# Optimization experiments

Hardware: AMD Instinct MI355X
Metric: run time of the kernel (lower is better)

Reference implementation:

```python
import jax, jax.numpy as jnp
import numpy as np

DIM = 4096  # hadamard_dim, power of 2 -> K=1, pure FWHT with 1/sqrt(n) scaling


def fwht(x):
    """Fast Walsh-Hadamard transform along the last axis, normalized by 1/sqrt(n).

    Butterfly network: log2(n) stages of pairwise add/sub. Matches the math of
    multiplying by the normalized n x n Hadamard matrix (x @ H / sqrt(n)).
    """
    orig_shape = x.shape
    n = orig_shape[-1]
    x = x.reshape(-1, n)
    h = 1
    while h < n:  # static unrolled loop over log2(n) stages (n is static)
        # view as [rows, n/(2h), 2, h]; butterfly pairs are (s=0, s=1)
        xb = x.reshape(-1, n // (2 * h), 2, h)
        a = xb[:, :, 0, :]
        b = xb[:, :, 1, :]
        x = jnp.stack([a + b, a - b], axis=2).reshape(-1, n)
        h *= 2
    scale = jnp.asarray(1.0 / np.sqrt(n), dtype=x.dtype)
    return (x * scale).reshape(orig_shape)


def setup_inputs() -> dict:
    key = jax.random.key(0)
    x = jax.random.normal(key, (4, 2048, DIM), dtype=jnp.float32)
    return {"x": x}


def reference(x):
    # force_fp32=True path: compute in fp32 (x already fp32), cast back to input dtype
    x_dtype = x.dtype
    y = fwht(x.astype(jnp.float32))
    return y.astype(x_dtype)
```

## Files before the change

kernel.cpp:

```cpp
#include <hip/hip_runtime.h>


using v4 = __attribute__((ext_vector_type(4))) float;
using u2 = __attribute__((ext_vector_type(2))) unsigned;

__device__ __forceinline__ void bfly_perm32(float& x, float& y) {
    u2 r = __builtin_amdgcn_permlane32_swap(__float_as_uint(x), __float_as_uint(y),
                                            false, false);
    float u = __uint_as_float(r[0]), v = __uint_as_float(r[1]);
    float s = u + v, d = u - v;
    u2 r2 = __builtin_amdgcn_permlane32_swap(__float_as_uint(s), __float_as_uint(d),
                                             false, false);
    x = __uint_as_float(r2[0]); y = __uint_as_float(r2[1]);
}

__device__ __forceinline__ void bfly_perm16(float& x, float& y) {
    u2 r = __builtin_amdgcn_permlane16_swap(__float_as_uint(x), __float_as_uint(y),
                                            false, false);
    float u = __uint_as_float(r[0]), v = __uint_as_float(r[1]);
    float s = u + v, d = u - v;
    u2 r2 = __builtin_amdgcn_permlane16_swap(__float_as_uint(s), __float_as_uint(d),
                                             false, false);
    x = __uint_as_float(r2[0]); y = __uint_as_float(r2[1]);
}

__device__ __forceinline__ void had16(float x[16]) {
#pragma unroll
    for (int h = 1; h < 16; h <<= 1) {
#pragma unroll
        for (int i = 0; i < 16; ++i) {
            if (!(i & h)) {
                float a = x[i], b = x[i ^ h];
                x[i] = a + b; x[i ^ h] = a - b;
            }
        }
    }
}

__global__ void __launch_bounds__(256) fwht4096_kernel(const float* __restrict__ in,
                                                       float* __restrict__ out) {
    __shared__ float lds[4096];
    const int t = threadIdx.x;
    const size_t base = (size_t)blockIdx.x * 4096;
    const v4* in4 = reinterpret_cast<const v4*>(in + base);
    v4* out4 = reinterpret_cast<v4*>(out + base);

    v4 v[4];
#pragma unroll
    for (int j = 0; j < 4; ++j) v[j] = __builtin_nontemporal_load(&in4[t + 256 * j]);

#pragma unroll
    for (int j = 0; j < 4; ++j) {
        float a = v[j][0], b = v[j][1], c = v[j][2], d = v[j][3];
        float ab = a + b, amb = a - b, cd = c + d, cmd = c - d;
        v[j][0] = ab + cd; v[j][1] = amb + cmd; v[j][2] = ab - cd; v[j][3] = amb - cmd;
    }
    {
        v4 s0 = v[0] + v[1], d0 = v[0] - v[1];
        v4 s1 = v[2] + v[3], d1 = v[2] - v[3];
        v[0] = s0 + s1; v[2] = s0 - s1;
        v[1] = d0 + d1; v[3] = d0 - d1;
    }
    {
#pragma unroll
        for (int e = 0; e < 4; ++e) {
            float a0 = v[0][e], a1 = v[1][e], a2 = v[2][e], a3 = v[3][e];
            bfly_perm16(a0, a1); bfly_perm16(a2, a3);
            bfly_perm32(a0, a1); bfly_perm32(a2, a3);
            v[0][e] = a0; v[1][e] = a1; v[2][e] = a2; v[3][e] = a3;
        }
    }
    {
        v4* l4 = reinterpret_cast<v4*>(lds);
        const int wb = t ^ ((t >> 4) & 7);
#pragma unroll
        for (int j = 0; j < 4; ++j) l4[wb + 256 * j] = v[j];
    }
    __syncthreads();

    {
        float x[16];
        const int b2 = (t & 3) + 64 * (t >> 2);
        const int s2 = (t >> 2) & 7;
#pragma unroll
        for (int r = 0; r < 16; ++r) x[r] = lds[b2 + 4 * (r ^ s2)];
        had16(x);
#pragma unroll
        for (int r = 0; r < 16; ++r) lds[b2 + 4 * (r ^ s2)] = x[r];
    }
    __syncthreads();

    {
        const v4* l4 = reinterpret_cast<const v4*>(lds);
        const int l = t & 63, w = t >> 6;
        v4 g[4];
#pragma unroll
        for (int m = 0; m < 4; ++m) {
            const int F = l + 64 * m + 256 * w;
            const int rb = F ^ ((F >> 4) & 7);
            g[m] = l4[rb];
        }
        v4 s0 = g[0] + g[1], d0 = g[0] - g[1];
        v4 s1 = g[2] + g[3], d1 = g[2] - g[3];
        const float scale = 0.015625f;
        out4[l + 256 * w]       = (s0 + s1) * scale;
        out4[l + 64 + 256 * w]  = (d0 + d1) * scale;
        out4[l + 128 + 256 * w] = (s0 - s1) * scale;
        out4[l + 192 + 256 * w] = (d0 - d1) * scale;
    }
}

extern "C" void kernel_launch(void* const* d_in, const int* in_sizes, int n_in,
                              void* d_out, int out_size, void* d_ws, size_t ws_size,
                              hipStream_t stream) {
    const float* x = (const float*)d_in[0];
    float* out = (float*)d_out;
    const int rows = in_sizes[0] >> 12;
    fwht4096_kernel<<<dim3(rows), dim3(256), 0, stream>>>(x, out);
}
```

Measured before the change: 219.1 us.

## Process four rows per block with register prefetch of next row

Each block now handles four consecutive rows, loading the next row into registers while the current row goes through the butterfly stages, and alternating between two LDS buffers. The output stores become nontemporal. The aim is to hide global load latency behind compute within a block. The cost is a quarter as many blocks (2048 for 8192 rows), higher register and LDS use per block, and a launch-bounds hint of 4 blocks per CU.

```diff
diff --git a/kernel.cpp b/kernel.cpp
--- a/kernel.cpp
+++ b/kernel.cpp
@@ -37,76 +37,92 @@
     }
 }
 
-__global__ void __launch_bounds__(256) fwht4096_kernel(const float* __restrict__ in,
-                                                       float* __restrict__ out) {
-    __shared__ float lds[4096];
+__global__ void __launch_bounds__(256, 4) fwht4096_kernel(const float* __restrict__ in,
+                                                          float* __restrict__ out,
+                                                          int rows) {
+    __shared__ float lds[2][4096];
     const int t = threadIdx.x;
-    const size_t base = (size_t)blockIdx.x * 4096;
-    const v4* in4 = reinterpret_cast<const v4*>(in + base);
-    v4* out4 = reinterpret_cast<v4*>(out + base);
+    const int row0 = blockIdx.x * 4;
+    const v4* in4 = reinterpret_cast<const v4*>(in) + (size_t)row0 * 1024;
+    v4* out4 = reinterpret_cast<v4*>(out) + (size_t)row0 * 1024;
 
-    v4 v[4];
+    v4 cur[4], nxt[4];
 #pragma unroll
-    for (int j = 0; j < 4; ++j) v[j] = __builtin_nontemporal_load(&in4[t + 256 * j]);
+    for (int j = 0; j < 4; ++j) cur[j] = __builtin_nontemporal_load(&in4[t + 256 * j]);
 
 #pragma unroll
-    for (int j = 0; j < 4; ++j) {
-        float a = v[j][0], b = v[j][1], c = v[j][2], d = v[j][3];
-        float ab = a + b, amb = a - b, cd = c + d, cmd = c - d;
-        v[j][0] = ab + cd; v[j][1] = amb + cmd; v[j][2] = ab - cd; v[j][3] = amb - cmd;
-    }
-    {
-        v4 s0 = v[0] + v[1], d0 = v[0] - v[1];
-        v4 s1 = v[2] + v[3], d1 = v[2] - v[3];
-        v[0] = s0 + s1; v[2] = s0 - s1;
-        v[1] = d0 + d1; v[3] = d0 - d1;
-    }
-    {
+    for (int r = 0; r < 4; ++r) {
+        if (row0 + r >= rows) break;
+
+        if (r < 3 && row0 + r + 1 < rows) {
+#pragma unroll
+            for (int j = 0; j < 4; ++j)
+                nxt[j] = __builtin_nontemporal_load(&in4[(r + 1) * 1024 + t + 256 * j]);
+        }
+
+#pragma unroll
+        for (int j = 0; j < 4; ++j) {
+            float a = cur[j][0], b = cur[j][1], c = cur[j][2], d = cur[j][3];
+            float ab = a + b, amb = a - b, cd = c + d, cmd = c - d;
+            cur[j][0] = ab + cd; cur[j][1] = amb + cmd;
+            cur[j][2] = ab - cd; cur[j][3] = amb - cmd;
+        }
+        {
+            v4 s0 = cur[0] + cur[1], d0 = cur[0] - cur[1];
+            v4 s1 = cur[2] + cur[3], d1 = cur[2] - cur[3];
+            cur[0] = s0 + s1; cur[2] = s0 - s1;
+            cur[1] = d0 + d1; cur[3] = d0 - d1;
+        }
 #pragma unroll
         for (int e = 0; e < 4; ++e) {
-            float a0 = v[0][e], a1 = v[1][e], a2 = v[2][e], a3 = v[3][e];
+            float a0 = cur[0][e], a1 = cur[1][e], a2 = cur[2][e], a3 = cur[3][e];
             bfly_perm16(a0, a1); bfly_perm16(a2, a3);
             bfly_perm32(a0, a1); bfly_perm32(a2, a3);
-            v[0][e] = a0; v[1][e] = a1; v[2][e] = a2; v[3][e] = a3;
+            cur[0][e] = a0; cur[1][e] = a1; cur[2][e] = a2; cur[3][e] = a3;
         }
-    }
-    {
-        v4* l4 = reinterpret_cast<v4*>(lds);
-        const int wb = t ^ ((t >> 4) & 7);
+        {
+            v4* l4 = reinterpret_cast<v4*>(lds[r & 1]);
+            const int wb = t ^ ((t >> 4) & 7);
 #pragma unroll
-        for (int j = 0; j < 4; ++j) l4[wb + 256 * j] = v[j];
-    }
-    __syncthreads();
+            for (int j = 0; j < 4; ++j) l4[wb + 256 * j] = cur[j];
+        }
+        __syncthreads();
 
-    {
-        float x[16];
-        const int b2 = (t & 3) + 64 * (t >> 2);
-        const int s2 = (t >> 2) & 7;
+        {
+            float x[16];
+            float* l = lds[r & 1];
+            const int b2 = (t & 3) + 64 * (t >> 2);
+            const int s2 = (t >> 2) & 7;
 #pragma unroll
-        for (int r = 0; r < 16; ++r) x[r] = lds[b2 + 4 * (r ^ s2)];
-        had16(x);
+            for (int q = 0; q < 16; ++q) x[q] = l[b2 + 4 * (q ^ s2)];
+            had16(x);
 #pragma unroll
-        for (int r = 0; r < 16; ++r) lds[b2 + 4 * (r ^ s2)] = x[r];
-    }
-    __syncthreads();
+            for (int q = 0; q < 16; ++q) l[b2 + 4 * (q ^ s2)] = x[q];
+        }
+        __syncthreads();
 
-    {
-        const v4* l4 = reinterpret_cast<const v4*>(lds);
-        const int l = t & 63, w = t >> 6;
-        v4 g[4];
+        {
+            const v4* l4 = reinterpret_cast<const v4*>(lds[r & 1]);
+            const int l = t & 63, w = t >> 6;
+            v4 g[4];
 #pragma unroll
-        for (int m = 0; m < 4; ++m) {
-            const int F = l + 64 * m + 256 * w;
-            const int rb = F ^ ((F >> 4) & 7);
-            g[m] = l4[rb];
+            for (int m = 0; m < 4; ++m) {
+                const int F = l + 64 * m + 256 * w;
+                const int rb = F ^ ((F >> 4) & 7);
+                g[m] = l4[rb];
+            }
+            v4 s0 = g[0] + g[1], d0 = g[0] - g[1];
+            v4 s1 = g[2] + g[3], d1 = g[2] - g[3];
+            const float scale = 0.015625f;
+            v4* o = out4 + r * 1024;
+            __builtin_nontemporal_store((s0 + s1) * scale, &o[l + 256 * w]);
+            __builtin_nontemporal_store((d0 + d1) * scale, &o[l + 64 + 256 * w]);
+            __builtin_nontemporal_store((s0 - s1) * scale, &o[l + 128 + 256 * w]);
+            __builtin_nontemporal_store((d0 - d1) * scale, &o[l + 192 + 256 * w]);
         }
-        v4 s0 = g[0] + g[1], d0 = g[0] - g[1];
-        v4 s1 = g[2] + g[3], d1 = g[2] - g[3];
-        const float scale = 0.015625f;
-        out4[l + 256 * w]       = (s0 + s1) * scale;
-        out4[l + 64 + 256 * w]  = (d0 + d1) * scale;
-        out4[l + 128 + 256 * w] = (s0 - s1) * scale;
-        out4[l + 192 + 256 * w] = (d0 - d1) * scale;
+
+#pragma unroll
+        for (int j = 0; j < 4; ++j) cur[j] = nxt[j];
     }
 }
 
@@ -116,5 +132,6 @@
     const float* x = (const float*)d_in[0];
     float* out = (float*)d_out;
     const int rows = in_sizes[0] >> 12;
-    fwht4096_kernel<<<dim3(rows), dim3(256), 0, stream>>>(x, out);
+    const int nb = (rows + 3) >> 2;
+    fwht4096_kernel<<<dim3(nb), dim3(256), 0, stream>>>(x, out, rows);
 }
```

Measured after the change: 221.5 us. No clear change (+1.1%).
